# Kernel optimization log

Measured on AMD Instinct MI355X. Metric: run time of the kernel, lower is better.

Reference implementation:

```python
import jax, jax.numpy as jnp
import numpy as np

LAYERS, BLOCKS = 10, 4
RES_CH, DIL_CH, SKIP_CH, CLASSES = 32, 32, 512, 256
K = 2                      # kernel_size
OUTPUT_LENGTH = 4096
N_LAYERS = LAYERS * BLOCKS
DILATIONS = [2 ** i for _ in range(BLOCKS) for i in range(LAYERS)]
BATCH, SEQ = 8, 8192       # SEQ divisible by max dilation 512; SEQ - 4092 >= OUTPUT_LENGTH


def conv1d(x, w, dilation=1):
    # x: (N, C_in, L), w: (C_out, C_in, K); causal valid dilated conv
    return jax.lax.conv_general_dilated(
        x, w, window_strides=(1,), padding='VALID',
        rhs_dilation=(dilation,), dimension_numbers=('NCH', 'OIH', 'NCH'))


def setup_inputs() -> dict:
    key = jax.random.key(0)
    ks = jax.random.split(key, 8)
    s = 0.1
    return {
        'x': jax.random.normal(ks[0], (BATCH, 1, SEQ), jnp.float32),
        'start_w': jax.random.normal(ks[1], (RES_CH, 1, 1), jnp.float32) * s,
        'filter_w': jax.random.normal(ks[2], (N_LAYERS, DIL_CH, RES_CH, K), jnp.float32) * s,
        'gate_w': jax.random.normal(ks[3], (N_LAYERS, DIL_CH, RES_CH, K), jnp.float32) * s,
        'res_w': jax.random.normal(ks[4], (N_LAYERS, RES_CH, DIL_CH, 1), jnp.float32) * s,
        'skip_w': jax.random.normal(ks[5], (N_LAYERS, SKIP_CH, DIL_CH, 1), jnp.float32) * s,
        'end_w': jax.random.normal(ks[6], (CLASSES, SKIP_CH, 1), jnp.float32) * s,
        'end_b': jax.random.normal(ks[7], (CLASSES,), jnp.float32) * s,
    }


def reference(x, start_w, filter_w, gate_w, res_w, skip_w, end_w, end_b):
    h = conv1d(x, start_w)                       # (N, RES_CH, SEQ)
    skip = None
    for i in range(N_LAYERS):
        d = DILATIONS[i]
        f = jnp.tanh(conv1d(h, filter_w[i], d))   # (N, DIL_CH, L - d*(K-1))
        g = jax.nn.sigmoid(conv1d(h, gate_w[i], d))
        z = f * g
        s = conv1d(z, skip_w[i])                  # (N, SKIP_CH, L')
        skip = s if skip is None else skip[:, :, -s.shape[2]:] + s
        h = conv1d(z, res_w[i]) + h[:, :, d * (K - 1):]
    out = conv1d(jax.nn.relu(skip), end_w) + end_b[None, :, None]
    out = out[:, :, -OUTPUT_LENGTH:]              # (N, CLASSES, OUTPUT_LENGTH)
    n, c, l = out.shape
    return out.transpose(0, 2, 1).reshape(n * l, c)
```

## Files before the change

kernel.cpp:

```cpp
#include <hip/hip_runtime.h>
#include <hip/hip_bf16.h>


#define BATCH   8
#define SEQ     8192
#define RES_CH  32
#define DIL_CH  32
#define SKIP_CH 512
#define CLASSES 256
#define NLAYERS 40
#define OUTLEN  4096
#define PSTART  (SEQ - OUTLEN)
#define QTOT    (NLAYERS * DIL_CH)

typedef __attribute__((ext_vector_type(8))) short bf16x8;
typedef __attribute__((ext_vector_type(4))) short short4_t;
typedef __attribute__((ext_vector_type(4))) float f32x4;

__device__ __forceinline__ short f2bf(float x) {
    __bf16 b = (__bf16)x;
    return __builtin_bit_cast(short, b);
}
__device__ __forceinline__ float bf2f(short s) {
    return __uint_as_float(((unsigned)(unsigned short)s) << 16);
}
__device__ __forceinline__ float zact(float f, float g) {
    float a = __expf(fminf(-2.0f * f, 80.0f));
    float b = __expf(fminf(-g, 80.0f));
    return (1.0f - a) * __builtin_amdgcn_rcpf((1.0f + a) * (1.0f + b));
}
__device__ __forceinline__ int tswz(int row, int cb) {
    return row * 64 + (cb ^ (((row & 3) << 4) | ((row & 4) << 3)));
}

#define GLOAD_LDS16(g, l)                                                    \
    __builtin_amdgcn_global_load_lds(                                        \
        (const __attribute__((address_space(1))) unsigned int*)(g),          \
        (__attribute__((address_space(3))) unsigned int*)(l), 16, 0, 0)

__global__ __launch_bounds__(256) void k_prep(
    const float* __restrict__ x, const float* __restrict__ sw,
    const float* __restrict__ fw, const float* __restrict__ gw,
    const float* __restrict__ rw, const float* __restrict__ wsk,
    const float* __restrict__ ew,
    float* __restrict__ hf, short* __restrict__ hb,
    short* __restrict__ wA, short* __restrict__ wR,
    short* __restrict__ wskB, short* __restrict__ ewB)
{
    const int gt = blockIdx.x * 256 + threadIdx.x;
    const int gn = gridDim.x * 256;
    for (int idx = gt; idx < BATCH * SEQ; idx += gn) {
        float v = x[idx];
        float* hp = hf + (size_t)idx * RES_CH;
        short* bp = hb + (size_t)idx * RES_CH;
#pragma unroll
        for (int c = 0; c < RES_CH; ++c) {
            float t = v * sw[c];
            hp[c] = t;
            bp[c] = f2bf(t);
        }
    }
    for (int idx = gt; idx < NLAYERS * 64 * 64; idx += gn) {
        int k = idx & 63, rho = (idx >> 6) & 63, i = idx >> 12;
        int tap = k >> 5, c = k & 31;
        int fgsel = rho >> 5, rr = rho & 31;
        int fp = rr >> 4, gg = (rr >> 2) & 3, e = rr & 3;
        int o = gg * 8 + fp * 4 + e;
        float v = fgsel ? gw[((i * 32 + o) * 32 + c) * 2 + tap]
                        : fw[((i * 32 + o) * 32 + c) * 2 + tap];
        wA[idx] = f2bf(v);
    }
    for (int idx = gt; idx < NLAYERS * 1024; idx += gn)
        wR[idx] = f2bf(rw[idx]);
    for (int idx = gt; idx < SKIP_CH * QTOT; idx += gn) {
        int s = idx / QTOT, q = idx - s * QTOT;
        int i = q >> 5, o = q & 31;
        wskB[idx] = f2bf(wsk[((size_t)i * SKIP_CH + s) * 32 + o]);
    }
    for (int idx = gt; idx < CLASSES * SKIP_CH; idx += gn)
        ewB[idx] = f2bf(ew[idx]);
}

template<bool OWNED>
__device__ __forceinline__ void chunk_body(
    int cp0, bool bglob, bool last, int d, int tog,
    const short* __restrict__ hbb, const float* __restrict__ hfb,
    float* __restrict__ hfo, short* __restrict__ hbo,
    short* __restrict__ zbb, int liq,
    const char* trd, char* tw,
    const bf16x8 (&av)[4][2], const bf16x8 (&avr)[2],
    f32x4 (*carryc)[2][2],
    int r, int g14)
{
    int pl[2]; bool pv[2];
#pragma unroll
    for (int fj = 0; fj < 2; ++fj) {
        int p = cp0 + fj * 16 + r;
        pv[fj] = p < SEQ;
        pl[fj] = pv[fj] ? p : SEQ - 1;
    }

    bf16x8 bv[2][2];
    if (bglob) {
#pragma unroll
        for (int fj = 0; fj < 2; ++fj) {
            bv[fj][0] = *(const bf16x8*)(hbb + (pl[fj] - d) * 32 + g14 * 8);
            bv[fj][1] = *(const bf16x8*)(hbb + pl[fj] * 32 + g14 * 8);
        }
    } else {
#pragma unroll
        for (int fj = 0; fj < 2; ++fj) {
            int tr = pl[fj] - tog;
            bv[fj][0] = *(const bf16x8*)(trd + tswz(tr - d, g14 * 16));
            bv[fj][1] = *(const bf16x8*)(trd + tswz(tr, g14 * 16));
        }
    }

    const f32x4 zero4 = {0.f, 0.f, 0.f, 0.f};
    f32x4 acc[4][2];
#pragma unroll
    for (int fi = 0; fi < 4; ++fi)
#pragma unroll
        for (int fj = 0; fj < 2; ++fj) acc[fi][fj] = zero4;
#pragma unroll
    for (int kt = 0; kt < 2; ++kt)
#pragma unroll
        for (int fi = 0; fi < 4; ++fi)
#pragma unroll
            for (int fj = 0; fj < 2; ++fj)
                acc[fi][fj] = __builtin_amdgcn_mfma_f32_16x16x32_bf16(
                    av[fi][kt], bv[fj][kt], acc[fi][fj], 0, 0, 0);

    bf16x8 zv8[2];
#pragma unroll
    for (int fj = 0; fj < 2; ++fj)
#pragma unroll
        for (int fp = 0; fp < 2; ++fp)
#pragma unroll
            for (int e = 0; e < 4; ++e)
                zv8[fj][fp * 4 + e] =
                    f2bf(zact(acc[fp][fj][e], acc[fp + 2][fj][e]));

    if constexpr (OWNED) {
#pragma unroll
        for (int fj = 0; fj < 2; ++fj)
            if (pv[fj] && pl[fj] >= PSTART) {
                short* zp = zbb + (size_t)(pl[fj] - PSTART) * QTOT + liq;
                *(bf16x8*)(zp + g14 * 8) = zv8[fj];
            }
    }

    f32x4 racc[2][2];
    if constexpr (OWNED) {
        if (bglob) {
#pragma unroll
            for (int fi = 0; fi < 2; ++fi)
#pragma unroll
                for (int fj = 0; fj < 2; ++fj)
                    racc[fi][fj] = *(const f32x4*)(hfb + pl[fj] * 32 + fi * 16 + g14 * 4);
        } else {
#pragma unroll
            for (int fi = 0; fi < 2; ++fi)
#pragma unroll
                for (int fj = 0; fj < 2; ++fj)
                    racc[fi][fj] = (*carryc)[fi][fj];
        }
    } else {
#pragma unroll
        for (int fj = 0; fj < 2; ++fj)
#pragma unroll
            for (int fi = 0; fi < 2; ++fi) {
                short4_t hv;
                if (bglob)
                    hv = *(const short4_t*)(hbb + pl[fj] * 32 + fi * 16 + g14 * 4);
                else
                    hv = *(const short4_t*)(trd + tswz(pl[fj] - tog, fi * 32 + g14 * 8));
                f32x4 cv;
#pragma unroll
                for (int e = 0; e < 4; ++e) cv[e] = bf2f(hv[e]);
                racc[fi][fj] = cv;
            }
    }

#pragma unroll
    for (int fi = 0; fi < 2; ++fi)
#pragma unroll
        for (int fj = 0; fj < 2; ++fj)
            racc[fi][fj] = __builtin_amdgcn_mfma_f32_16x16x32_bf16(
                avr[fi], zv8[fj], racc[fi][fj], 0, 0, 0);

    if constexpr (OWNED) {
#pragma unroll
        for (int fi = 0; fi < 2; ++fi)
#pragma unroll
            for (int fj = 0; fj < 2; ++fj)
                (*carryc)[fi][fj] = racc[fi][fj];
    }

    if (!last) {
#pragma unroll
        for (int fj = 0; fj < 2; ++fj)
            if (pv[fj]) {
                int tr = pl[fj] - tog;
#pragma unroll
                for (int fi = 0; fi < 2; ++fi) {
                    short4_t sv;
#pragma unroll
                    for (int e = 0; e < 4; ++e) sv[e] = f2bf(racc[fi][fj][e]);
                    *(short4_t*)(tw + tswz(tr, fi * 32 + g14 * 8)) = sv;
                }
            }
    } else {
        if constexpr (OWNED) {
#pragma unroll
            for (int fj = 0; fj < 2; ++fj)
                if (pv[fj]) {
#pragma unroll
                    for (int fi = 0; fi < 2; ++fi) {
                        *(f32x4*)(hfo + pl[fj] * 32 + fi * 16 + g14 * 4) = racc[fi][fj];
                        short4_t sv;
#pragma unroll
                        for (int e = 0; e < 4; ++e) sv[e] = f2bf(racc[fi][fj][e]);
                        *(short4_t*)(hbo + pl[fj] * 32 + fi * 16 + g14 * 4) = sv;
                    }
                }
        }
    }
}

template<int LC, int S, int TH, int NTB>
__global__ __launch_bounds__(512, 2) void k_fused8(
    const float* __restrict__ hfin, const short* __restrict__ hbin,
    float* __restrict__ hfout, short* __restrict__ hbout,
    const short* __restrict__ wAg, const short* __restrict__ wRg,
    short* __restrict__ Z, int li0, int pminIn, int hsum, int segbase)
{
    constexpr int TROWS = TH + S;
    __shared__ short tile[NTB][TROWS][32];

    const int lane = threadIdx.x & 63;
    const int w    = threadIdx.x >> 6;
    const int r = lane & 15, g14 = lane >> 4;
    const int b = blockIdx.y;
    const int seg0 = segbase + blockIdx.x * S;
    const int tog  = seg0 - TH;

    const float* hfb = hfin + (size_t)b * SEQ * RES_CH;
    const short* hbb = hbin + (size_t)b * SEQ * RES_CH;
    float* hfo = hfout + (size_t)b * SEQ * RES_CH;
    short* hbo = hbout + (size_t)b * SEQ * RES_CH;
    short* zbb = Z + (size_t)b * OUTLEN * QTOT;

    f32x4 carry[2][2];
    int Ht = hsum, pmt = pminIn;

#pragma unroll 1
    for (int t = 0; t < LC; ++t) {
        const int d = 1 << ((li0 + t) % 10);
        Ht -= d; pmt += d;
        const bool bglob = (t == 0);
        const bool last  = (t == LC - 1);
        const short* wAl = wAg + (li0 + t) * 4096;
        const short* wRl = wRg + (li0 + t) * 1024;
        const int liq = (li0 + t) * DIL_CH;
        char* tw = (char*)&tile[t & (NTB - 1)][0][0];
        const char* trd = (const char*)&tile[(t + NTB - 1) & (NTB - 1)][0][0];

        bf16x8 av[4][2];
#pragma unroll
        for (int fi = 0; fi < 4; ++fi)
#pragma unroll
            for (int kt = 0; kt < 2; ++kt)
                av[fi][kt] = *(const bf16x8*)(wAl + (fi * 16 + r) * 64 + kt * 32 + g14 * 8);
        bf16x8 avr[2];
#pragma unroll
        for (int fi = 0; fi < 2; ++fi)
            avr[fi] = *(const bf16x8*)(wRl + (fi * 16 + r) * 32 + g14 * 8);

        {
            const int cp0 = seg0 + w * 32;
            chunk_body<true>(cp0, bglob, last, d, tog, hbb, hfb, hfo, hbo,
                             zbb, liq, trd, tw, av, avr, &carry, r, g14);
        }
        int lo = seg0 - Ht; if (lo < pmt) lo = pmt;
        const int nh = (seg0 - lo + 31) >> 5;
#pragma unroll 1
        for (int hc = w; hc < nh; hc += 8) {
            const int cp0 = seg0 - (hc + 1) * 32;
            chunk_body<false>(cp0, bglob, last, d, tog, hbb, hfb, hfo, hbo,
                              zbb, liq, trd, tw, av, avr, nullptr, r, g14);
        }
        __syncthreads();
    }
}

__global__ __launch_bounds__(512, 1) void k_skip_8ph(
    const short* __restrict__ Z, const short* __restrict__ wskB,
    short* __restrict__ skipb)
{
    __shared__ short lds[2][32768];

    const int bid = blockIdx.x;
    const int b   = bid & 7;
    const int sb  = (bid >> 3) & 1;
    const int pb  = bid >> 4;
    const int s0  = sb * 256;
    const int p0  = pb * 256;

    const int tid  = threadIdx.x;
    const int lane = tid & 63;
    const int w    = tid >> 6;
    const int wm   = w >> 2;
    const int wn   = w & 3;
    const int r = lane & 15, g = lane >> 4;

    const short* Ag = wskB + (size_t)s0 * QTOT;
    const short* Bg = Z + ((size_t)b * OUTLEN + p0) * QTOT;

    const int srow = tid >> 3;
    const int sblk = tid & 7;

#define STG(PI, ISA, HH, KT)                                                  \
    {                                                                         \
        _Pragma("unroll") for (int j = 0; j < 2; ++j) {                       \
            int grow = (HH) * 128 + j * 64 + srow;                            \
            const short* gp = ((ISA) ? Ag : Bg) + (size_t)grow * QTOT         \
                              + (KT) * 64 + ((sblk ^ (grow & 7)) * 8);        \
            short* lp = &lds[PI][((ISA) ? 0 : 16384) +                        \
                                 ((HH) * 128 + j * 64 + w * 8) * 64];         \
            GLOAD_LDS16(gp, lp);                                              \
        }                                                                     \
    }

#define DS_A(dst, bufi, fi_, kk_)                                             \
    { int row_ = wm * 128 + (fi_) * 16 + r;                                   \
      dst = *(const bf16x8*)&lds[bufi][row_ * 64 + ((((kk_) * 4 + g) ^ (row_ & 7)) * 8)]; }
#define DS_B(dst, bufi, fj_, kk_)                                             \
    { int row_ = wn * 64 + (fj_) * 16 + r;                                    \
      dst = *(const bf16x8*)&lds[bufi][16384 + row_ * 64 + ((((kk_) * 4 + g) ^ (row_ & 7)) * 8)]; }

#define FENCE asm volatile("" ::: "memory")
#define VM4   asm volatile("s_waitcnt vmcnt(4)" ::: "memory")

#define PHASE(BUF, FIB, READB, STAGECODE, VMW)                                \
    {                                                                         \
        if (READB) {                                                          \
            _Pragma("unroll") for (int fj = 0; fj < 4; ++fj)                  \
                _Pragma("unroll") for (int kk = 0; kk < 2; ++kk)              \
                    DS_B(bv[fj][kk], BUF, fj, kk);                            \
        }                                                                     \
        bf16x8 a0k0, a0k1, a1k0, a1k1;                                        \
        DS_A(a0k0, BUF, FIB, 0); DS_A(a0k1, BUF, FIB, 1);                     \
        DS_A(a1k0, BUF, (FIB) + 1, 0); DS_A(a1k1, BUF, (FIB) + 1, 1);         \
        STAGECODE;                                                            \
        VMW;                                                                  \
        FENCE; __builtin_amdgcn_s_barrier(); FENCE;                           \
        __builtin_amdgcn_s_setprio(1);                                        \
        _Pragma("unroll") for (int fj = 0; fj < 4; ++fj) {                    \
            acc[FIB][fj] = __builtin_amdgcn_mfma_f32_16x16x32_bf16(           \
                a0k0, bv[fj][0], acc[FIB][fj], 0, 0, 0);                      \
            acc[FIB][fj] = __builtin_amdgcn_mfma_f32_16x16x32_bf16(           \
                a0k1, bv[fj][1], acc[FIB][fj], 0, 0, 0);                      \
            acc[(FIB) + 1][fj] = __builtin_amdgcn_mfma_f32_16x16x32_bf16(     \
                a1k0, bv[fj][0], acc[(FIB) + 1][fj], 0, 0, 0);                \
            acc[(FIB) + 1][fj] = __builtin_amdgcn_mfma_f32_16x16x32_bf16(     \
                a1k1, bv[fj][1], acc[(FIB) + 1][fj], 0, 0, 0);                \
        }                                                                     \
        __builtin_amdgcn_s_setprio(0);                                        \
        FENCE; __builtin_amdgcn_s_barrier(); FENCE;                           \
    }

    f32x4 acc[8][4];
    const f32x4 zero4 = {0.f, 0.f, 0.f, 0.f};
#pragma unroll
    for (int fi = 0; fi < 8; ++fi)
#pragma unroll
        for (int fj = 0; fj < 4; ++fj) acc[fi][fj] = zero4;

    bf16x8 bv[4][2];

    STG(0, 1, 0, 0) STG(0, 1, 1, 0) STG(0, 0, 0, 0) STG(0, 0, 1, 0)
    STG(1, 0, 0, 1) STG(1, 0, 1, 1)
    VM4;
    FENCE; __builtin_amdgcn_s_barrier(); FENCE;

    const int NIT = QTOT / 128;
#pragma unroll 1
    for (int i = 0; i < NIT; ++i) {
        const int k1 = 2 * i + 1;
        const int k2 = 2 * i + 2, k3 = 2 * i + 3;
        const bool more = (i + 1 < NIT);
        PHASE(0, 0, 1, STG(1, 1, 0, k1), )
        PHASE(0, 2, 0, STG(1, 1, 1, k1), )
        PHASE(0, 4, 0, if (more) STG(0, 0, 0, k2), )
        PHASE(0, 6, 0, if (more) STG(0, 0, 1, k2), VM4)
        PHASE(1, 0, 1, if (more) STG(0, 1, 0, k2), )
        PHASE(1, 2, 0, if (more) STG(0, 1, 1, k2), )
        PHASE(1, 4, 0, if (more) STG(1, 0, 0, k3), )
        PHASE(1, 6, 0, if (more) STG(1, 0, 1, k3), VM4)
    }

    short* skb = skipb + (size_t)b * OUTLEN * SKIP_CH;
#pragma unroll
    for (int fj = 0; fj < 4; ++fj) {
        int p = p0 + wn * 64 + fj * 16 + r;
#pragma unroll
        for (int fi = 0; fi < 8; ++fi) {
            int s = s0 + wm * 128 + fi * 16 + g * 4;
            short4_t v;
#pragma unroll
            for (int e = 0; e < 4; ++e) v[e] = f2bf(fmaxf(acc[fi][fj][e], 0.f));
            *(short4_t*)(skb + (size_t)p * SKIP_CH + s) = v;
        }
    }
#undef PHASE
#undef STG
#undef DS_A
#undef DS_B
}

#define EK_STAGE(bf, kt)                                                      \
    {                                                                         \
        _Pragma("unroll") for (int j = 0; j < 2; ++j) {                       \
            const short* ga = Ab + (size_t)(rb + j * 16 + l4) * SKIP_CH       \
                                 + (kt) * 32 + csw * 8;                       \
            GLOAD_LDS16(ga, &At[bf][(rb + j * 16) * 32]);                     \
            const short* gb = Bb + (size_t)(rb + j * 16 + l4) * SKIP_CH       \
                                 + (kt) * 32 + csw * 8;                       \
            GLOAD_LDS16(gb, &Bt[bf][(rb + j * 16) * 32]);                     \
        }                                                                     \
    }

__global__ __launch_bounds__(256) void k_end_m97(
    const short* __restrict__ skipB, const short* __restrict__ ewB,
    const float* __restrict__ eb, float* __restrict__ out)
{
    __shared__ short At[2][128 * 32];
    __shared__ short Bt[2][128 * 32];

    const int bid = blockIdx.x;
    const int b    = bid & 7;
    const int rest = bid >> 3;
    const int cb   = rest & 1;
    const int pb   = rest >> 1;
    const int c0   = cb * 128;
    const int p0   = pb * 128;

    const int lane = threadIdx.x & 63;
    const int w    = threadIdx.x >> 6;
    const int r = lane & 15, g14 = lane >> 4;
    const int soff = (w >> 1) * 64;
    const int poff = (w & 1) * 64;

    const short* Ab = ewB + (size_t)c0 * SKIP_CH;
    const short* Bb = skipB + ((size_t)b * OUTLEN + p0) * SKIP_CH;

    const int rb = w * 32;
    const int l4 = lane >> 2;
    const int c4 = lane & 3;
    const int csw = c4 ^ ((l4 >> 1) & 3);
    const int rsw = (g14 ^ ((r >> 1) & 3)) * 8;

    f32x4 acc[4][4];
    const f32x4 zero4 = {0.f, 0.f, 0.f, 0.f};
#pragma unroll
    for (int fi = 0; fi < 4; ++fi)
#pragma unroll
        for (int fj = 0; fj < 4; ++fj) acc[fi][fj] = zero4;

    EK_STAGE(0, 0)
    __syncthreads();

    int cur = 0;
#pragma unroll 1
    for (int kt = 0; kt < SKIP_CH / 32; ++kt) {
        if (kt + 1 < SKIP_CH / 32) EK_STAGE(cur ^ 1, kt + 1)

        bf16x8 av[4], bv[4];
#pragma unroll
        for (int fi = 0; fi < 4; ++fi)
            av[fi] = *(const bf16x8*)&At[cur][(soff + fi * 16 + r) * 32 + rsw];
#pragma unroll
        for (int fj = 0; fj < 4; ++fj)
            bv[fj] = *(const bf16x8*)&Bt[cur][(poff + fj * 16 + r) * 32 + rsw];

#pragma unroll
        for (int fi = 0; fi < 4; ++fi)
#pragma unroll
            for (int fj = 0; fj < 4; ++fj)
                acc[fi][fj] = __builtin_amdgcn_mfma_f32_16x16x32_bf16(
                    av[fi], bv[fj], acc[fi][fj], 0, 0, 0);

        __syncthreads();
        cur ^= 1;
    }

#pragma unroll
    for (int fj = 0; fj < 4; ++fj) {
        int p = p0 + poff + fj * 16 + r;
#pragma unroll
        for (int fi = 0; fi < 4; ++fi) {
            int cls = c0 + soff + fi * 16 + g14 * 4;
            f32x4 bias = *(const f32x4*)(eb + cls);
            f32x4 v;
#pragma unroll
            for (int e = 0; e < 4; ++e) v[e] = acc[fi][fj][e] + bias[e];
            *(f32x4*)(out + ((size_t)b * OUTLEN + p) * CLASSES + cls) = v;
        }
    }
}

extern "C" void kernel_launch(void* const* d_in, const int* in_sizes, int n_in,
                              void* d_out, int out_size, void* d_ws, size_t ws_size,
                              hipStream_t stream) {
    const float* x   = (const float*)d_in[0];
    const float* sw  = (const float*)d_in[1];
    const float* fw  = (const float*)d_in[2];
    const float* gw  = (const float*)d_in[3];
    const float* rw  = (const float*)d_in[4];
    const float* wsk = (const float*)d_in[5];
    const float* ew  = (const float*)d_in[6];
    const float* eb  = (const float*)d_in[7];
    float* out = (float*)d_out;

    const size_t HN = (size_t)BATCH * SEQ * RES_CH;
    float* hf0 = (float*)d_ws;
    float* hf1 = hf0 + HN;
    short* hb0 = (short*)(hf1 + HN);
    short* hb1 = hb0 + HN;
    short* Z     = hb1 + HN;
    short* skipb = Z + (size_t)BATCH * OUTLEN * QTOT;
    short* wA    = skipb + (size_t)BATCH * OUTLEN * SKIP_CH;
    short* wR    = wA + NLAYERS * 64 * 64;
    short* wskB  = wR + NLAYERS * 32 * 32;
    short* ewB   = wskB + (size_t)SKIP_CH * QTOT;

    k_prep<<<dim3(1024), 256, 0, stream>>>(x, sw, fw, gw, rw, wsk, ew,
                                           hf0, hb0, wA, wR, wskB, ewB);

    float* hf[2] = {hf0, hf1};
    short* hb[2] = {hb0, hb1};
    int cur = 0, pmin = 0;
    for (int dec = 0; dec < 4; ++dec) {
        int li0 = dec * 10;
        int segbase = pmin + 255;
        int nseg = (SEQ - segbase + 255) / 256;
        k_fused8<8, 256, 288, 2><<<dim3(nseg, BATCH), 512, 0, stream>>>(
            hf[cur], hb[cur], hf[cur ^ 1], hb[cur ^ 1], wA, wR, Z,
            li0, pmin, 255, segbase);
        cur ^= 1; pmin = segbase;
        segbase = pmin + 768;
        nseg = (SEQ - segbase + 255) / 256;
        k_fused8<2, 256, 512, 1><<<dim3(nseg, BATCH), 512, 0, stream>>>(
            hf[cur], hb[cur], hf[cur ^ 1], hb[cur ^ 1], wA, wR, Z,
            li0 + 8, pmin, 768, segbase);
        cur ^= 1; pmin = segbase;
    }

    k_skip_8ph<<<dim3(256), 512, 0, stream>>>(Z, wskB, skipb);
    k_end_m97<<<dim3(512), 256, 0, stream>>>(skipb, ewB, eb, out);
}
```

Measured before the change: 304.0 us.

## Split fused layer kernel into 16-wide chunks across 16 waves per block

The fused dilated-conv layer kernel now runs 1024 threads per block, and each wave handles 16 sequence positions instead of 32. This halves per-wave register state (accumulators, carry) so more waves can overlap MFMA latency and the activation math. The block barrier is replaced with an inline-asm LDS waitcnt plus s_barrier, which avoids waiting on outstanding global memory operations. Each wave now issues half as many MFMAs per weight load, and more waves contend for the LDS tile. Boundary clamping of positions is also tightened.

New measurement: 350.3 us. +15.2%, slower.

```diff
diff --git a/kernel.cpp b/kernel.cpp
--- a/kernel.cpp
+++ b/kernel.cpp
@@ -31,6 +31,9 @@
 }
 __device__ __forceinline__ int tswz(int row, int cb) {
     return row * 64 + (cb ^ (((row & 3) << 4) | ((row & 4) << 3)));
+}
+__device__ __forceinline__ void lgkm_barrier() {
+    asm volatile("s_waitcnt lgkmcnt(0)\n\ts_barrier" ::: "memory");
 }
 
 #define GLOAD_LDS16(g, l)                                                    \
@@ -82,154 +85,118 @@
 }
 
 template<bool OWNED>
-__device__ __forceinline__ void chunk_body(
+__device__ __forceinline__ void chunk16(
     int cp0, bool bglob, bool last, int d, int tog,
     const short* __restrict__ hbb, const float* __restrict__ hfb,
     float* __restrict__ hfo, short* __restrict__ hbo,
     short* __restrict__ zbb, int liq,
     const char* trd, char* tw,
     const bf16x8 (&av)[4][2], const bf16x8 (&avr)[2],
-    f32x4 (*carryc)[2][2],
+    f32x4 (*carryc)[2],
     int r, int g14)
 {
-    int pl[2]; bool pv[2];
-#pragma unroll
-    for (int fj = 0; fj < 2; ++fj) {
-        int p = cp0 + fj * 16 + r;
-        pv[fj] = p < SEQ;
-        pl[fj] = pv[fj] ? p : SEQ - 1;
-    }
-
-    bf16x8 bv[2][2];
+    const int p = cp0 + r;
+    const bool pv = (unsigned)p < SEQ;
+    int pl = p < 0 ? 0 : (p >= SEQ ? SEQ - 1 : p);
+    int pm = pl - d; if (pm < 0) pm = 0;
+
+    bf16x8 bv0, bv1;
     if (bglob) {
-#pragma unroll
-        for (int fj = 0; fj < 2; ++fj) {
-            bv[fj][0] = *(const bf16x8*)(hbb + (pl[fj] - d) * 32 + g14 * 8);
-            bv[fj][1] = *(const bf16x8*)(hbb + pl[fj] * 32 + g14 * 8);
-        }
+        bv0 = *(const bf16x8*)(hbb + pm * 32 + g14 * 8);
+        bv1 = *(const bf16x8*)(hbb + pl * 32 + g14 * 8);
     } else {
-#pragma unroll
-        for (int fj = 0; fj < 2; ++fj) {
-            int tr = pl[fj] - tog;
-            bv[fj][0] = *(const bf16x8*)(trd + tswz(tr - d, g14 * 16));
-            bv[fj][1] = *(const bf16x8*)(trd + tswz(tr, g14 * 16));
-        }
+        int tr = pl - tog;
+        bv0 = *(const bf16x8*)(trd + tswz(tr - d, g14 * 16));
+        bv1 = *(const bf16x8*)(trd + tswz(tr, g14 * 16));
     }
 
     const f32x4 zero4 = {0.f, 0.f, 0.f, 0.f};
-    f32x4 acc[4][2];
+    f32x4 acc[4];
+#pragma unroll
+    for (int fi = 0; fi < 4; ++fi) acc[fi] = zero4;
 #pragma unroll
     for (int fi = 0; fi < 4; ++fi)
-#pragma unroll
-        for (int fj = 0; fj < 2; ++fj) acc[fi][fj] = zero4;
-#pragma unroll
-    for (int kt = 0; kt < 2; ++kt)
-#pragma unroll
-        for (int fi = 0; fi < 4; ++fi)
-#pragma unroll
-            for (int fj = 0; fj < 2; ++fj)
-                acc[fi][fj] = __builtin_amdgcn_mfma_f32_16x16x32_bf16(
-                    av[fi][kt], bv[fj][kt], acc[fi][fj], 0, 0, 0);
-
-    bf16x8 zv8[2];
-#pragma unroll
-    for (int fj = 0; fj < 2; ++fj)
-#pragma unroll
-        for (int fp = 0; fp < 2; ++fp)
-#pragma unroll
-            for (int e = 0; e < 4; ++e)
-                zv8[fj][fp * 4 + e] =
-                    f2bf(zact(acc[fp][fj][e], acc[fp + 2][fj][e]));
+        acc[fi] = __builtin_amdgcn_mfma_f32_16x16x32_bf16(av[fi][0], bv0, acc[fi], 0, 0, 0);
+#pragma unroll
+    for (int fi = 0; fi < 4; ++fi)
+        acc[fi] = __builtin_amdgcn_mfma_f32_16x16x32_bf16(av[fi][1], bv1, acc[fi], 0, 0, 0);
+
+    bf16x8 zv8;
+#pragma unroll
+    for (int fp = 0; fp < 2; ++fp)
+#pragma unroll
+        for (int e = 0; e < 4; ++e)
+            zv8[fp * 4 + e] = f2bf(zact(acc[fp][e], acc[fp + 2][e]));
 
     if constexpr (OWNED) {
-#pragma unroll
-        for (int fj = 0; fj < 2; ++fj)
-            if (pv[fj] && pl[fj] >= PSTART) {
-                short* zp = zbb + (size_t)(pl[fj] - PSTART) * QTOT + liq;
-                *(bf16x8*)(zp + g14 * 8) = zv8[fj];
-            }
-    }
-
-    f32x4 racc[2][2];
+        if (pv && pl >= PSTART)
+            *(bf16x8*)(zbb + (size_t)(pl - PSTART) * QTOT + liq + g14 * 8) = zv8;
+    }
+
+    f32x4 racc[2];
     if constexpr (OWNED) {
         if (bglob) {
 #pragma unroll
             for (int fi = 0; fi < 2; ++fi)
-#pragma unroll
-                for (int fj = 0; fj < 2; ++fj)
-                    racc[fi][fj] = *(const f32x4*)(hfb + pl[fj] * 32 + fi * 16 + g14 * 4);
+                racc[fi] = *(const f32x4*)(hfb + pl * 32 + fi * 16 + g14 * 4);
         } else {
 #pragma unroll
             for (int fi = 0; fi < 2; ++fi)
-#pragma unroll
-                for (int fj = 0; fj < 2; ++fj)
-                    racc[fi][fj] = (*carryc)[fi][fj];
+                racc[fi] = (*carryc)[fi];
         }
     } else {
 #pragma unroll
-        for (int fj = 0; fj < 2; ++fj)
+        for (int fi = 0; fi < 2; ++fi) {
+            short4_t hv;
+            if (bglob)
+                hv = *(const short4_t*)(hbb + pl * 32 + fi * 16 + g14 * 4);
+            else
+                hv = *(const short4_t*)(trd + tswz(pl - tog, fi * 32 + g14 * 8));
+            f32x4 cv;
+#pragma unroll
+            for (int e = 0; e < 4; ++e) cv[e] = bf2f(hv[e]);
+            racc[fi] = cv;
+        }
+    }
+
+#pragma unroll
+    for (int fi = 0; fi < 2; ++fi)
+        racc[fi] = __builtin_amdgcn_mfma_f32_16x16x32_bf16(avr[fi], zv8, racc[fi], 0, 0, 0);
+
+    if constexpr (OWNED) {
+#pragma unroll
+        for (int fi = 0; fi < 2; ++fi) (*carryc)[fi] = racc[fi];
+    }
+
+    if (!last) {
+        if (pv) {
+            int tr = pl - tog;
 #pragma unroll
             for (int fi = 0; fi < 2; ++fi) {
-                short4_t hv;
-                if (bglob)
-                    hv = *(const short4_t*)(hbb + pl[fj] * 32 + fi * 16 + g14 * 4);
-                else
-                    hv = *(const short4_t*)(trd + tswz(pl[fj] - tog, fi * 32 + g14 * 8));
-                f32x4 cv;
-#pragma unroll
-                for (int e = 0; e < 4; ++e) cv[e] = bf2f(hv[e]);
-                racc[fi][fj] = cv;
+                short4_t sv;
+#pragma unroll
+                for (int e = 0; e < 4; ++e) sv[e] = f2bf(racc[fi][e]);
+                *(short4_t*)(tw + tswz(tr, fi * 32 + g14 * 8)) = sv;
             }
-    }
-
-#pragma unroll
-    for (int fi = 0; fi < 2; ++fi)
-#pragma unroll
-        for (int fj = 0; fj < 2; ++fj)
-            racc[fi][fj] = __builtin_amdgcn_mfma_f32_16x16x32_bf16(
-                avr[fi], zv8[fj], racc[fi][fj], 0, 0, 0);
-
-    if constexpr (OWNED) {
-#pragma unroll
-        for (int fi = 0; fi < 2; ++fi)
-#pragma unroll
-            for (int fj = 0; fj < 2; ++fj)
-                (*carryc)[fi][fj] = racc[fi][fj];
-    }
-
-    if (!last) {
-#pragma unroll
-        for (int fj = 0; fj < 2; ++fj)
-            if (pv[fj]) {
-                int tr = pl[fj] - tog;
+        }
+    } else {
+        if constexpr (OWNED) {
+            if (pv) {
 #pragma unroll
                 for (int fi = 0; fi < 2; ++fi) {
+                    *(f32x4*)(hfo + pl * 32 + fi * 16 + g14 * 4) = racc[fi];
                     short4_t sv;
 #pragma unroll
-                    for (int e = 0; e < 4; ++e) sv[e] = f2bf(racc[fi][fj][e]);
-                    *(short4_t*)(tw + tswz(tr, fi * 32 + g14 * 8)) = sv;
+                    for (int e = 0; e < 4; ++e) sv[e] = f2bf(racc[fi][e]);
+                    *(short4_t*)(hbo + pl * 32 + fi * 16 + g14 * 4) = sv;
                 }
             }
-    } else {
-        if constexpr (OWNED) {
-#pragma unroll
-            for (int fj = 0; fj < 2; ++fj)
-                if (pv[fj]) {
-#pragma unroll
-                    for (int fi = 0; fi < 2; ++fi) {
-                        *(f32x4*)(hfo + pl[fj] * 32 + fi * 16 + g14 * 4) = racc[fi][fj];
-                        short4_t sv;
-#pragma unroll
-                        for (int e = 0; e < 4; ++e) sv[e] = f2bf(racc[fi][fj][e]);
-                        *(short4_t*)(hbo + pl[fj] * 32 + fi * 16 + g14 * 4) = sv;
-                    }
-                }
         }
     }
 }
 
 template<int LC, int S, int TH, int NTB>
-__global__ __launch_bounds__(512, 2) void k_fused8(
+__global__ __launch_bounds__(1024, 4) void k_fused16(
     const float* __restrict__ hfin, const short* __restrict__ hbin,
     float* __restrict__ hfout, short* __restrict__ hbout,
     const short* __restrict__ wAg, const short* __restrict__ wRg,
@@ -251,7 +218,7 @@
     short* hbo = hbout + (size_t)b * SEQ * RES_CH;
     short* zbb = Z + (size_t)b * OUTLEN * QTOT;
 
-    f32x4 carry[2][2];
+    f32x4 carry[2];
     int Ht = hsum, pmt = pminIn;
 
 #pragma unroll 1
@@ -278,19 +245,19 @@
             avr[fi] = *(const bf16x8*)(wRl + (fi * 16 + r) * 32 + g14 * 8);
 
         {
-            const int cp0 = seg0 + w * 32;
-            chunk_body<true>(cp0, bglob, last, d, tog, hbb, hfb, hfo, hbo,
-                             zbb, liq, trd, tw, av, avr, &carry, r, g14);
+            const int cp0 = seg0 + w * 16;
+            chunk16<true>(cp0, bglob, last, d, tog, hbb, hfb, hfo, hbo,
+                          zbb, liq, trd, tw, av, avr, &carry, r, g14);
         }
         int lo = seg0 - Ht; if (lo < pmt) lo = pmt;
-        const int nh = (seg0 - lo + 31) >> 5;
+        const int nh = (seg0 - lo + 15) >> 4;
 #pragma unroll 1
-        for (int hc = w; hc < nh; hc += 8) {
-            const int cp0 = seg0 - (hc + 1) * 32;
-            chunk_body<false>(cp0, bglob, last, d, tog, hbb, hfb, hfo, hbo,
-                              zbb, liq, trd, tw, av, avr, nullptr, r, g14);
-        }
-        __syncthreads();
+        for (int hc = w; hc < nh; hc += 16) {
+            const int cp0 = seg0 - (hc + 1) * 16;
+            chunk16<false>(cp0, bglob, last, d, tog, hbb, hfb, hfo, hbo,
+                           zbb, liq, trd, tw, av, avr, nullptr, r, g14);
+        }
+        lgkm_barrier();
     }
 }
 
@@ -545,13 +512,13 @@
         int li0 = dec * 10;
         int segbase = pmin + 255;
         int nseg = (SEQ - segbase + 255) / 256;
-        k_fused8<8, 256, 288, 2><<<dim3(nseg, BATCH), 512, 0, stream>>>(
+        k_fused16<8, 256, 288, 2><<<dim3(nseg, BATCH), 1024, 0, stream>>>(
             hf[cur], hb[cur], hf[cur ^ 1], hb[cur ^ 1], wA, wR, Z,
             li0, pmin, 255, segbase);
         cur ^= 1; pmin = segbase;
         segbase = pmin + 768;
         nseg = (SEQ - segbase + 255) / 256;
-        k_fused8<2, 256, 512, 1><<<dim3(nseg, BATCH), 512, 0, stream>>>(
+        k_fused16<2, 256, 512, 1><<<dim3(nseg, BATCH), 1024, 0, stream>>>(
             hf[cur], hb[cur], hf[cur ^ 1], hb[cur ^ 1], wA, wR, Z,
             li0 + 8, pmin, 768, segbase);
         cur ^= 1; pmin = segbase;
```
